# Performance work log

Hardware: AMD Instinct MI355X
Metric: run time of the kernel (lower is better)

Reference implementation:

```python
import jax, jax.numpy as jnp
import numpy as np

HDIM = 1024
N_CLASSES = 50257
CUTOFFS = [2000, 10000, N_CLASSES]  # shortlist=2000, clusters: [2000,10000), [10000,50257)
DIV = 4.0
HEAD_SIZE = CUTOFFS[0] + 2  # shortlist + 2 cluster logits


def setup_inputs() -> dict:
    key = jax.random.key(0)
    ks = jax.random.split(key, 12)
    B, S, K = 8, 512, 256
    N = B * K
    hsz0 = int(HDIM // (DIV ** 1))  # 256
    hsz1 = int(HDIM // (DIV ** 2))  # 64
    osz0 = CUTOFFS[1] - CUTOFFS[0]  # 8000
    osz1 = CUTOFFS[2] - CUTOFFS[1]  # 40257
    w = 0.02
    return {
        "targets": jax.random.randint(ks[0], (N,), 0, N_CLASSES),
        "last_hidden_states": jax.random.normal(ks[1], (B, S, HDIM), dtype=jnp.float32),
        "cls_tokens_batch": jax.random.normal(ks[2], (B, HDIM), dtype=jnp.float32),
        "idx": jax.random.randint(ks[3], (B, K), 0, S),
        "head_W": jax.random.normal(ks[4], (HEAD_SIZE, HDIM), dtype=jnp.float32) * w,
        "head_b": jnp.zeros((HEAD_SIZE,), dtype=jnp.float32),
        "proj0_W": jax.random.normal(ks[5], (hsz0, HDIM), dtype=jnp.float32) * w,
        "out0_W": jax.random.normal(ks[6], (osz0, hsz0), dtype=jnp.float32) * w,
        "proj1_W": jax.random.normal(ks[7], (hsz1, HDIM), dtype=jnp.float32) * w,
        "out1_W": jax.random.normal(ks[8], (osz1, hsz1), dtype=jnp.float32) * w,
    }


def reference(targets, last_hidden_states, cls_tokens_batch, idx,
              head_W, head_b, proj0_W, out0_W, proj1_W, out1_W):
    # Gather context token embeddings: [B, K, H] -> [N, H]
    B, S, H = last_hidden_states.shape
    x = last_hidden_states[jnp.arange(B)[:, None], idx].reshape(-1, H)
    N = x.shape[0]
    c0, c1 = CUTOFFS[0], CUTOFFS[1]

    # Head: shortlist logits + per-cluster routing logits, [N, c0+2]
    head_logprob = jax.nn.log_softmax(x @ head_W.T + head_b, axis=-1)
    # Tail clusters: low-rank projection then output GEMM + log-softmax
    lp0 = jax.nn.log_softmax((x @ proj0_W.T) @ out0_W.T, axis=-1)  # [N, 8000]
    lp1 = jax.nn.log_softmax((x @ proj1_W.T) @ out1_W.T, axis=-1)  # [N, 40257]

    n = jnp.arange(N)
    t = targets
    short = head_logprob[n, jnp.clip(t, 0, c0 - 1)]
    mid = head_logprob[:, c0] + lp0[n, jnp.clip(t - c0, 0, lp0.shape[1] - 1)]
    high = head_logprob[:, c0 + 1] + lp1[n, jnp.clip(t - c1, 0, lp1.shape[1] - 1)]
    out = jnp.where(t < c0, short, jnp.where(t < c1, mid, high))  # target log-probs [N]
    loss = -jnp.mean(out)
    return out, loss
```

## Files before the change

### kernel.cpp

```cpp
#include <hip/hip_runtime.h>
#include <hip/hip_bf16.h>

#define NROWS 2048
#define L2E 1.4426950408889634f

typedef float f32x4 __attribute__((ext_vector_type(4)));
typedef __bf16 bf16x8 __attribute__((ext_vector_type(8)));
typedef short s16x8 __attribute__((ext_vector_type(8)));

typedef const __attribute__((address_space(1))) unsigned int* gas_t;
typedef __attribute__((address_space(3))) unsigned int* las_t;

__device__ __forceinline__ unsigned short f2bf(float f) {
    unsigned int u = __float_as_uint(f);
    unsigned int r = (u + 0x7FFFu + ((u >> 16) & 1u)) >> 16;
    return (unsigned short)r;
}
__device__ __forceinline__ float bf2f(unsigned short u) {
    return __uint_as_float((unsigned int)u << 16);
}
__device__ __forceinline__ f32x4 mfma16(s16x8 a, s16x8 b, f32x4 c) {
    return __builtin_amdgcn_mfma_f32_16x16x32_bf16(
        __builtin_bit_cast(bf16x8, a), __builtin_bit_cast(bf16x8, b), c, 0, 0, 0);
}

__global__ void k_prologue(const float* __restrict__ lhs, const int* __restrict__ idx,
                           const float* __restrict__ hw, const float* __restrict__ p0w,
                           const float* __restrict__ p1w, const float* __restrict__ o0w,
                           const float* __restrict__ o1w, const float* __restrict__ hb,
                           const int* __restrict__ tgt,
                           unsigned short* __restrict__ xb, unsigned short* __restrict__ hWb,
                           unsigned short* __restrict__ pW01, unsigned short* __restrict__ o0Wb,
                           unsigned short* __restrict__ o1Wb,
                           float* __restrict__ bias_s, int* __restrict__ tc) {
    int bid = blockIdx.x;
    if (bid < 2048) {
        int tid = bid * 256 + threadIdx.x;
        int n = tid >> 8;
        int c = (tid & 255) << 2;
        int b = n >> 8, k = n & 255;
        int srow = idx[(b << 8) + k];
        const float4 v = *reinterpret_cast<const float4*>(
            lhs + (((size_t)b << 9) + srow) * 1024 + c);
        ushort4 o = make_ushort4(f2bf(v.x), f2bf(v.y), f2bf(v.z), f2bf(v.w));
        *reinterpret_cast<ushort4*>(xb + (size_t)n * 1024 + c) = o;
        return;
    }
    bid -= 2048;
    if (bid < 6968) {
        const long B0 = 2048L * 1024;
        const long B1 = B0 + 384L * 1024;
        const long B2 = B1 + 8064L * 256;
        const long B3 = B2 + 40320L * 64;
        long e = ((long)bid * 256 + threadIdx.x) * 4;
        if (e >= B3) return;
        const float* src; unsigned short* dst; long rows; int colshift; long base;
        float sc;
        if (e < B0)      { base = 0;  src = hw;  dst = hWb;  rows = 2002;  colshift = 10; sc = L2E; }
        else if (e < B1) {
            long l = e - B0;
            long row = l >> 10;
            unsigned short* d = pW01 + l;
            ushort4 o;
            if (row < 256) {
                float4 v = *reinterpret_cast<const float4*>(p0w + l);
                o = make_ushort4(f2bf(v.x), f2bf(v.y), f2bf(v.z), f2bf(v.w));
            } else if (row < 320) {
                float4 v = *reinterpret_cast<const float4*>(p1w + (l - 256L * 1024));
                o = make_ushort4(f2bf(v.x), f2bf(v.y), f2bf(v.z), f2bf(v.w));
            } else {
                o = make_ushort4(0, 0, 0, 0);
            }
            *reinterpret_cast<ushort4*>(d) = o;
            return;
        }
        else if (e < B2) { base = B1; src = o0w; dst = o0Wb; rows = 8000;  colshift = 8; sc = L2E; }
        else             { base = B2; src = o1w; dst = o1Wb; rows = 40257; colshift = 6; sc = L2E; }
        long l = e - base;
        long row = l >> colshift;
        ushort4 o;
        if (row < rows) {
            float4 v = *reinterpret_cast<const float4*>(src + l);
            o = make_ushort4(f2bf(v.x * sc), f2bf(v.y * sc), f2bf(v.z * sc), f2bf(v.w * sc));
        } else {
            o = make_ushort4(0, 0, 0, 0);
        }
        *reinterpret_cast<ushort4*>(dst + l) = o;
        return;
    }
    bid -= 6968;
    int n = bid * 256 + threadIdx.x;
    if (n >= 2048) return;
    bias_s[n] = (n < 2002) ? hb[n] * L2E : -1e30f;
    int t = tgt[n];
    tc[n] = min(t, 1999);
    tc[2048 + n] = min(max(t - 2000, 0), 7999);
    tc[4096 + n] = min(max(t - 10000, 0), 40256);
}

template <int NT>
__global__ __launch_bounds__(256)
void k_mm(const unsigned short* __restrict__ A, int lda,
          const unsigned short* __restrict__ B, int ldb,
          const float* __restrict__ bias, float* __restrict__ partial,
          unsigned short* __restrict__ hout, int hstride, int hcols, int fsplit) {
    __shared__ unsigned short As[2][128 * 64];
    __shared__ unsigned short Bs[2][128 * 64];
    const int tid = threadIdx.x;
    const int lane = tid & 63, wid = tid >> 6;
    const int wr = wid >> 1, wc = wid & 1;
    const int g = lane >> 4, cl = lane & 15;
    const int row0 = blockIdx.x * 128;
    const int col0 = blockIdx.y * 128;

    const int sr = wid * 8 + (lane >> 3);
    const int swz = ((lane & 7) ^ (lane >> 3)) * 8;
    const unsigned short* Ab = A + (size_t)(row0 + sr) * lda + swz;
    const unsigned short* Bb = B + (size_t)(col0 + sr) * ldb + swz;

    auto stage = [&](int buf, int kt) {
        const unsigned short* ga = Ab + kt;
        const unsigned short* gb = Bb + kt;
        unsigned short* la = &As[buf][wid * 8 * 64];
        unsigned short* lb = &Bs[buf][wid * 8 * 64];
#pragma unroll
        for (int i = 0; i < 4; ++i) {
            __builtin_amdgcn_global_load_lds((gas_t)(const void*)(ga + (size_t)i * 32 * lda),
                                             (las_t)(void*)(la + i * 32 * 64), 16, 0, 0);
            __builtin_amdgcn_global_load_lds((gas_t)(const void*)(gb + (size_t)i * 32 * ldb),
                                             (las_t)(void*)(lb + i * 32 * 64), 16, 0, 0);
        }
    };

    f32x4 acc[4][4] = {};
    stage(0, 0);
    asm volatile("s_waitcnt vmcnt(0)" ::: "memory");
    __builtin_amdgcn_s_barrier();
    const int sA = (cl & 7);
    for (int t = 0; t < NT; ++t) {
        if (t + 1 < NT) stage((t + 1) & 1, (t + 1) * 64);
        const unsigned short* Al = &As[t & 1][(wr * 64 + cl) * 64];
        const unsigned short* Bl = &Bs[t & 1][(wc * 64 + cl) * 64];
#pragma unroll
        for (int kk2 = 0; kk2 < 2; ++kk2) {
            const int slot = ((kk2 * 4 + g) ^ sA) * 8;
            s16x8 a[4], b[4];
#pragma unroll
            for (int mi = 0; mi < 4; ++mi)
                a[mi] = *reinterpret_cast<const s16x8*>(Al + mi * 16 * 64 + slot);
#pragma unroll
            for (int ni = 0; ni < 4; ++ni)
                b[ni] = *reinterpret_cast<const s16x8*>(Bl + ni * 16 * 64 + slot);
#pragma unroll
            for (int mi = 0; mi < 4; ++mi)
#pragma unroll
                for (int ni = 0; ni < 4; ++ni)
                    acc[mi][ni] = mfma16(a[mi], b[ni], acc[mi][ni]);
        }
        if (t + 1 < NT) {
            asm volatile("s_waitcnt vmcnt(0)" ::: "memory");
            __builtin_amdgcn_s_barrier();
        }
    }

    if ((int)blockIdx.y >= fsplit) {
        int c0 = col0 - fsplit * 128;
#pragma unroll
        for (int mi = 0; mi < 4; ++mi)
#pragma unroll
            for (int ni = 0; ni < 4; ++ni) {
                int col = c0 + wc * 64 + ni * 16 + cl;
                if (col < hcols) {
#pragma unroll
                    for (int r = 0; r < 4; ++r) {
                        int row = row0 + wr * 64 + mi * 16 + g * 4 + r;
                        hout[(size_t)row * hstride + col] = f2bf(acc[mi][ni][r]);
                    }
                }
            }
    } else {
        float bv[4];
#pragma unroll
        for (int ni = 0; ni < 4; ++ni)
            bv[ni] = bias ? bias[col0 + wc * 64 + ni * 16 + cl] : 0.f;
        int strip = blockIdx.y * 2 + wc;
#pragma unroll
        for (int mi = 0; mi < 4; ++mi)
#pragma unroll
            for (int r = 0; r < 4; ++r) {
                float s = 0.f;
#pragma unroll
                for (int ni = 0; ni < 4; ++ni)
                    s += __builtin_amdgcn_exp2f(acc[mi][ni][r] + bv[ni]);
                s += __shfl_xor(s, 1, 64);
                s += __shfl_xor(s, 2, 64);
                s += __shfl_xor(s, 4, 64);
                s += __shfl_xor(s, 8, 64);
                if (cl == 0)
                    partial[(size_t)strip * NROWS + row0 + wr * 64 + mi * 16 + g * 4 + r] = s;
            }
    }
}

#define OUT1_IT 5
__global__ __launch_bounds__(256, 4)
void k_out1(const unsigned short* __restrict__ h01, const unsigned short* __restrict__ B,
            float* __restrict__ p1) {
    __shared__ unsigned short Bs[2][128 * 64];
    const int tid = threadIdx.x;
    const int lane = tid & 63, wid = tid >> 6;
    const int wr = wid >> 1, wc = wid & 1;
    const int g = lane >> 4, cl = lane & 15;
    const int row0 = blockIdx.x * 128 + wr * 64;
    const int t0 = blockIdx.y * OUT1_IT;

    s16x8 a[4][2];
#pragma unroll
    for (int mi = 0; mi < 4; ++mi)
#pragma unroll
        for (int kk = 0; kk < 2; ++kk)
            a[mi][kk] = *reinterpret_cast<const s16x8*>(
                h01 + (size_t)(row0 + mi * 16 + cl) * 320 + 256 + kk * 32 + g * 8);

    const int sr = wid * 8 + (lane >> 3);
    const int swz = ((lane & 7) ^ (lane >> 3)) * 8;
    auto stage = [&](int buf, int tile) {
        const unsigned short* gb = B + ((size_t)tile * 128 + sr) * 64 + swz;
        unsigned short* lb = &Bs[buf][wid * 8 * 64];
#pragma unroll
        for (int i = 0; i < 4; ++i)
            __builtin_amdgcn_global_load_lds((gas_t)(const void*)(gb + (size_t)i * 32 * 64),
                                             (las_t)(void*)(lb + i * 32 * 64), 16, 0, 0);
    };

    float sexp[4][4] = {};
    const f32x4 z4 = {0.f, 0.f, 0.f, 0.f};
    stage(0, t0);
    asm volatile("s_waitcnt vmcnt(0)" ::: "memory");
    __builtin_amdgcn_s_barrier();
    int buf = 0;
    const int sA = (cl & 7);
#pragma unroll 1
    for (int it = 0; it < OUT1_IT; ++it) {
        if (it + 1 < OUT1_IT) stage(buf ^ 1, t0 + it + 1);
        const unsigned short* Bl = Bs[buf];
#pragma unroll
        for (int ni = 0; ni < 4; ++ni) {
            const unsigned short* br = Bl + (wc * 64 + ni * 16 + cl) * 64;
            s16x8 b0 = *reinterpret_cast<const s16x8*>(br + (g ^ sA) * 8);
            s16x8 b1 = *reinterpret_cast<const s16x8*>(br + ((4 + g) ^ sA) * 8);
            f32x4 acc[4];
#pragma unroll
            for (int mi = 0; mi < 4; ++mi)
                acc[mi] = mfma16(a[mi][0], b0, z4);
#pragma unroll
            for (int mi = 0; mi < 4; ++mi)
                acc[mi] = mfma16(a[mi][1], b1, acc[mi]);
#pragma unroll
            for (int mi = 0; mi < 4; ++mi)
#pragma unroll
                for (int r = 0; r < 4; ++r)
                    sexp[mi][r] += __builtin_amdgcn_exp2f(acc[mi][r]);
        }
        if (it + 1 < OUT1_IT) {
            asm volatile("s_waitcnt vmcnt(0)" ::: "memory");
            __builtin_amdgcn_s_barrier();
            buf ^= 1;
        }
    }

#pragma unroll
    for (int mi = 0; mi < 4; ++mi)
#pragma unroll
        for (int r = 0; r < 4; ++r) {
            float s = sexp[mi][r];
            s += __shfl_xor(s, 1, 64);
            s += __shfl_xor(s, 2, 64);
            s += __shfl_xor(s, 4, 64);
            s += __shfl_xor(s, 8, 64);
            if (cl == 0)
                p1[(size_t)(blockIdx.y * 2 + wc) * NROWS + row0 + mi * 16 + g * 4 + r] = s;
        }
}

__global__ __launch_bounds__(256)
void k_dots(const unsigned short* __restrict__ xb, const unsigned short* __restrict__ h01,
            const float* __restrict__ headW, const float* __restrict__ hb,
            const float* __restrict__ o0w, const float* __restrict__ o1w,
            const int* __restrict__ tc,
            float* __restrict__ tgh, float* __restrict__ r0, float* __restrict__ r1,
            float* __restrict__ tg0, float* __restrict__ tg1) {
    int lane = threadIdx.x & 63;
    int n = (blockIdx.x * 256 + threadIdx.x) >> 6;
    int tch = tc[n], tc0 = tc[2048 + n], tc1 = tc[4096 + n];
    const unsigned short* xr = xb + (size_t)n * 1024 + lane * 16;
    s16x8 x0 = *reinterpret_cast<const s16x8*>(xr);
    s16x8 x1 = *reinterpret_cast<const s16x8*>(xr + 8);
    const float* wh = headW + (size_t)tch * 1024 + lane * 16;
    const float* wa = headW + (size_t)2000 * 1024 + lane * 16;
    const float* wb = headW + (size_t)2001 * 1024 + lane * 16;
    float dh = 0.f, da = 0.f, db = 0.f;
#pragma unroll
    for (int i = 0; i < 8; ++i) {
        float xv = bf2f((unsigned short)x0[i]);
        dh += xv * wh[i]; da += xv * wa[i]; db += xv * wb[i];
    }
#pragma unroll
    for (int i = 0; i < 8; ++i) {
        float xv = bf2f((unsigned short)x1[i]);
        dh += xv * wh[8 + i]; da += xv * wa[8 + i]; db += xv * wb[8 + i];
    }
    ushort4 h0v = *reinterpret_cast<const ushort4*>(h01 + (size_t)n * 320 + lane * 4);
    float4 w0v = *reinterpret_cast<const float4*>(o0w + (size_t)tc0 * 256 + lane * 4);
    float d2 = bf2f(h0v.x) * w0v.x + bf2f(h0v.y) * w0v.y +
               bf2f(h0v.z) * w0v.z + bf2f(h0v.w) * w0v.w;
    float d3 = bf2f(h01[(size_t)n * 320 + 256 + lane]) * o1w[(size_t)tc1 * 64 + lane];
#pragma unroll
    for (int m = 1; m < 64; m <<= 1) {
        dh += __shfl_xor(dh, m, 64);
        da += __shfl_xor(da, m, 64);
        db += __shfl_xor(db, m, 64);
        d2 += __shfl_xor(d2, m, 64);
        d3 += __shfl_xor(d3, m, 64);
    }
    if (lane == 0) {
        tgh[n] = dh + hb[tch];
        r0[n] = da + hb[2000];
        r1[n] = db + hb[2001];
        tg0[n] = d2;
        tg1[n] = d3;
    }
}

__global__ void k_finalize(const float* __restrict__ ph, const float* __restrict__ p0,
                           const float* __restrict__ p1, const float* __restrict__ tgh,
                           const float* __restrict__ r0, const float* __restrict__ r1,
                           const float* __restrict__ tg0, const float* __restrict__ tg1,
                           const int* __restrict__ tgt, float* __restrict__ outv,
                           float* __restrict__ bsum) {
    int n = blockIdx.x * 128 + threadIdx.x;
    float sh = 0.f, s0 = 0.f, s1 = 0.f;
    for (int s = 0; s < 32; ++s) sh += ph[(size_t)s * NROWS + n];
    for (int s = 0; s < 126; ++s) s0 += p0[(size_t)s * NROWS + n];
    for (int s = 0; s < 126; ++s) s1 += p1[(size_t)s * NROWS + n];
    s0 -= 64.f;
    s1 -= 63.f;
    float lh = __logf(sh), l0 = __logf(s0), l1 = __logf(s1);
    int t = tgt[n];
    float o;
    if (t < 2000) o = tgh[n] - lh;
    else if (t < 10000) o = (r0[n] - lh) + (tg0[n] - l0);
    else o = (r1[n] - lh) + (tg1[n] - l1);
    outv[n] = o;
    __shared__ float red[128];
    red[threadIdx.x] = o;
    __syncthreads();
    for (int s = 64; s > 0; s >>= 1) {
        if (threadIdx.x < s) red[threadIdx.x] += red[threadIdx.x + s];
        __syncthreads();
    }
    if (threadIdx.x == 0) bsum[blockIdx.x] = red[0];
}

__global__ void k_loss(const float* __restrict__ bsum, float* __restrict__ loss) {
    float s = 0.f;
    for (int i = 0; i < 16; ++i) s += bsum[i];
    *loss = -s / (float)NROWS;
}

extern "C" void kernel_launch(void* const* d_in, const int* in_sizes, int n_in,
                              void* d_out, int out_size, void* d_ws, size_t ws_size,
                              hipStream_t stream) {
    const int* targets   = (const int*)d_in[0];
    const float* lhs     = (const float*)d_in[1];
    const int* idx       = (const int*)d_in[3];
    const float* head_W  = (const float*)d_in[4];
    const float* head_b  = (const float*)d_in[5];
    const float* proj0_W = (const float*)d_in[6];
    const float* out0_W  = (const float*)d_in[7];
    const float* proj1_W = (const float*)d_in[8];
    const float* out1_W  = (const float*)d_in[9];

    char* ws = (char*)d_ws;
    size_t off = 0;
    auto alloc = [&](size_t bytes) -> void* {
        void* p = ws + off;
        off += (bytes + 255) & ~(size_t)255;
        return p;
    };

    unsigned short* xb   = (unsigned short*)alloc((size_t)2048 * 1024 * 2);
    unsigned short* wB   = (unsigned short*)alloc((size_t)2432 * 1024 * 2);
    unsigned short* hWb  = wB;
    unsigned short* pW01 = wB + (size_t)2048 * 1024;
    unsigned short* o0Wb = (unsigned short*)alloc((size_t)8064 * 256 * 2);
    unsigned short* o1Wb = (unsigned short*)alloc((size_t)40320 * 64 * 2);
    unsigned short* h01  = (unsigned short*)alloc((size_t)2048 * 320 * 2);
    float* ph  = (float*)alloc((size_t)32 * 2048 * 4);
    float* p0  = (float*)alloc((size_t)126 * 2048 * 4);
    float* p1  = (float*)alloc((size_t)126 * 2048 * 4);
    float* tgh = (float*)alloc(2048 * 4);
    float* r0  = (float*)alloc(2048 * 4);
    float* r1  = (float*)alloc(2048 * 4);
    float* tg0 = (float*)alloc(2048 * 4);
    float* tg1 = (float*)alloc(2048 * 4);
    int*   tc  = (int*)alloc(3 * 2048 * 4);
    float* bias_s = (float*)alloc(2048 * 4);
    float* bsum = (float*)alloc(16 * 4);

    k_prologue<<<9024, 256, 0, stream>>>(lhs, idx, head_W, proj0_W, proj1_W, out0_W, out1_W,
                                         head_b, targets,
                                         xb, hWb, pW01, o0Wb, o1Wb, bias_s, tc);

    k_mm<16><<<dim3(16, 19), 256, 0, stream>>>(
        xb, 1024, wB, 1024, bias_s, ph, h01, 320, 320, 16);
    k_mm<4><<<dim3(16, 63), 256, 0, stream>>>(
        h01, 320, o0Wb, 256, nullptr, p0, nullptr, 0, 0, 63);
    k_out1<<<dim3(16, 63), 256, 0, stream>>>(h01, o1Wb, p1);

    k_dots<<<512, 256, 0, stream>>>(xb, h01, head_W, head_b, out0_W, out1_W, tc,
                                    tgh, r0, r1, tg0, tg1);

    float* outv = (float*)d_out;
    float* loss = (float*)d_out + NROWS;
    k_finalize<<<16, 128, 0, stream>>>(ph, p0, p1, tgh, r0, r1, tg0, tg1, targets, outv, bsum);
    k_loss<<<1, 1, 0, stream>>>(bsum, loss);
}
```

Measured before the change: 92.39 us.

## Merge out0 GEMM, out1 GEMM and target-dot kernels into one launch

Three independent kernels (the cluster-0 GEMM with exp-sum, the cluster-1 GEMM with exp-sum, and the per-row target dot products) become a single kernel that dispatches on block index into three roles. This removes two launch gaps and lets the three workloads' blocks run concurrently, filling the GPU better than three serial launches with tails. In exchange the merged kernel uses 32 KB of shared memory and the register budget of the heaviest branch, and the launch-bounds occupancy hint of 4 blocks per SM is dropped, which may lower occupancy for the out1 path.

```diff
diff --git a/kernel.cpp b/kernel.cpp
--- a/kernel.cpp
+++ b/kernel.cpp
@@ -203,95 +203,163 @@
 }
 
 #define OUT1_IT 5
-__global__ __launch_bounds__(256, 4)
-void k_out1(const unsigned short* __restrict__ h01, const unsigned short* __restrict__ B,
-            float* __restrict__ p1) {
-    __shared__ unsigned short Bs[2][128 * 64];
+__global__ __launch_bounds__(256)
+void k_tail(const unsigned short* __restrict__ h01, const unsigned short* __restrict__ o0Wb,
+            const unsigned short* __restrict__ o1Wb, const unsigned short* __restrict__ xb,
+            const float* __restrict__ headW, const float* __restrict__ hb,
+            const float* __restrict__ o0w, const float* __restrict__ o1w,
+            const int* __restrict__ tc,
+            float* __restrict__ p0, float* __restrict__ p1,
+            float* __restrict__ tgh, float* __restrict__ r0, float* __restrict__ r1,
+            float* __restrict__ tg0, float* __restrict__ tg1) {
+    __shared__ unsigned short smem[4][128 * 64];
     const int tid = threadIdx.x;
     const int lane = tid & 63, wid = tid >> 6;
     const int wr = wid >> 1, wc = wid & 1;
     const int g = lane >> 4, cl = lane & 15;
-    const int row0 = blockIdx.x * 128 + wr * 64;
-    const int t0 = blockIdx.y * OUT1_IT;
-
-    s16x8 a[4][2];
-#pragma unroll
-    for (int mi = 0; mi < 4; ++mi)
-#pragma unroll
-        for (int kk = 0; kk < 2; ++kk)
-            a[mi][kk] = *reinterpret_cast<const s16x8*>(
-                h01 + (size_t)(row0 + mi * 16 + cl) * 320 + 256 + kk * 32 + g * 8);
-
-    const int sr = wid * 8 + (lane >> 3);
-    const int swz = ((lane & 7) ^ (lane >> 3)) * 8;
-    auto stage = [&](int buf, int tile) {
-        const unsigned short* gb = B + ((size_t)tile * 128 + sr) * 64 + swz;
-        unsigned short* lb = &Bs[buf][wid * 8 * 64];
-#pragma unroll
-        for (int i = 0; i < 4; ++i)
-            __builtin_amdgcn_global_load_lds((gas_t)(const void*)(gb + (size_t)i * 32 * 64),
-                                             (las_t)(void*)(lb + i * 32 * 64), 16, 0, 0);
-    };
-
-    float sexp[4][4] = {};
-    const f32x4 z4 = {0.f, 0.f, 0.f, 0.f};
-    stage(0, t0);
-    asm volatile("s_waitcnt vmcnt(0)" ::: "memory");
-    __builtin_amdgcn_s_barrier();
-    int buf = 0;
-    const int sA = (cl & 7);
+    int bid = blockIdx.x;
+
+    if (bid < 1008) {
+        const int row0 = (bid & 15) * 128;
+        const int col0 = (bid >> 4) * 128;
+        const int sr = wid * 8 + (lane >> 3);
+        const int swz = ((lane & 7) ^ (lane >> 3)) * 8;
+        const unsigned short* Ab = h01 + (size_t)(row0 + sr) * 320 + swz;
+        const unsigned short* Bb = o0Wb + (size_t)(col0 + sr) * 256 + swz;
+        auto stage = [&](int buf, int kt) {
+            const unsigned short* ga = Ab + kt;
+            const unsigned short* gb = Bb + kt;
+            unsigned short* la = &smem[buf][wid * 8 * 64];
+            unsigned short* lb = &smem[2 + buf][wid * 8 * 64];
+#pragma unroll
+            for (int i = 0; i < 4; ++i) {
+                __builtin_amdgcn_global_load_lds((gas_t)(const void*)(ga + (size_t)i * 32 * 320),
+                                                 (las_t)(void*)(la + i * 32 * 64), 16, 0, 0);
+                __builtin_amdgcn_global_load_lds((gas_t)(const void*)(gb + (size_t)i * 32 * 256),
+                                                 (las_t)(void*)(lb + i * 32 * 64), 16, 0, 0);
+            }
+        };
+        f32x4 acc[4][4] = {};
+        stage(0, 0);
+        asm volatile("s_waitcnt vmcnt(0)" ::: "memory");
+        __builtin_amdgcn_s_barrier();
+        const int sA = (cl & 7);
+        for (int t = 0; t < 4; ++t) {
+            if (t < 3) stage((t + 1) & 1, (t + 1) * 64);
+            const unsigned short* Al = &smem[t & 1][(wr * 64 + cl) * 64];
+            const unsigned short* Bl = &smem[2 + (t & 1)][(wc * 64 + cl) * 64];
+#pragma unroll
+            for (int kk2 = 0; kk2 < 2; ++kk2) {
+                const int slot = ((kk2 * 4 + g) ^ sA) * 8;
+                s16x8 a[4], b[4];
+#pragma unroll
+                for (int mi = 0; mi < 4; ++mi)
+                    a[mi] = *reinterpret_cast<const s16x8*>(Al + mi * 16 * 64 + slot);
+#pragma unroll
+                for (int ni = 0; ni < 4; ++ni)
+                    b[ni] = *reinterpret_cast<const s16x8*>(Bl + ni * 16 * 64 + slot);
+#pragma unroll
+                for (int mi = 0; mi < 4; ++mi)
+#pragma unroll
+                    for (int ni = 0; ni < 4; ++ni)
+                        acc[mi][ni] = mfma16(a[mi], b[ni], acc[mi][ni]);
+            }
+            if (t < 3) {
+                asm volatile("s_waitcnt vmcnt(0)" ::: "memory");
+                __builtin_amdgcn_s_barrier();
+            }
+        }
+        int strip = (bid >> 4) * 2 + wc;
+#pragma unroll
+        for (int mi = 0; mi < 4; ++mi)
+#pragma unroll
+            for (int r = 0; r < 4; ++r) {
+                float s = 0.f;
+#pragma unroll
+                for (int ni = 0; ni < 4; ++ni)
+                    s += __builtin_amdgcn_exp2f(acc[mi][ni][r]);
+                s += __shfl_xor(s, 1, 64);
+                s += __shfl_xor(s, 2, 64);
+                s += __shfl_xor(s, 4, 64);
+                s += __shfl_xor(s, 8, 64);
+                if (cl == 0)
+                    p0[(size_t)strip * NROWS + row0 + wr * 64 + mi * 16 + g * 4 + r] = s;
+            }
+        return;
+    }
+    if (bid < 2016) {
+        bid -= 1008;
+        const int row0 = (bid & 15) * 128 + wr * 64;
+        const int yb = bid >> 4;
+        const int t0 = yb * OUT1_IT;
+        s16x8 a[4][2];
+#pragma unroll
+        for (int mi = 0; mi < 4; ++mi)
+#pragma unroll
+            for (int kk = 0; kk < 2; ++kk)
+                a[mi][kk] = *reinterpret_cast<const s16x8*>(
+                    h01 + (size_t)(row0 + mi * 16 + cl) * 320 + 256 + kk * 32 + g * 8);
+        const int sr = wid * 8 + (lane >> 3);
+        const int swz = ((lane & 7) ^ (lane >> 3)) * 8;
+        auto stage = [&](int buf, int tile) {
+            const unsigned short* gb = o1Wb + ((size_t)tile * 128 + sr) * 64 + swz;
+            unsigned short* lb = &smem[buf][wid * 8 * 64];
+#pragma unroll
+            for (int i = 0; i < 4; ++i)
+                __builtin_amdgcn_global_load_lds((gas_t)(const void*)(gb + (size_t)i * 32 * 64),
+                                                 (las_t)(void*)(lb + i * 32 * 64), 16, 0, 0);
+        };
+        float sexp[4][4] = {};
+        const f32x4 z4 = {0.f, 0.f, 0.f, 0.f};
+        stage(0, t0);
+        asm volatile("s_waitcnt vmcnt(0)" ::: "memory");
+        __builtin_amdgcn_s_barrier();
+        int buf = 0;
+        const int sA = (cl & 7);
 #pragma unroll 1
-    for (int it = 0; it < OUT1_IT; ++it) {
-        if (it + 1 < OUT1_IT) stage(buf ^ 1, t0 + it + 1);
-        const unsigned short* Bl = Bs[buf];
-#pragma unroll
-        for (int ni = 0; ni < 4; ++ni) {
-            const unsigned short* br = Bl + (wc * 64 + ni * 16 + cl) * 64;
-            s16x8 b0 = *reinterpret_cast<const s16x8*>(br + (g ^ sA) * 8);
-            s16x8 b1 = *reinterpret_cast<const s16x8*>(br + ((4 + g) ^ sA) * 8);
-            f32x4 acc[4];
-#pragma unroll
-            for (int mi = 0; mi < 4; ++mi)
-                acc[mi] = mfma16(a[mi][0], b0, z4);
-#pragma unroll
-            for (int mi = 0; mi < 4; ++mi)
-                acc[mi] = mfma16(a[mi][1], b1, acc[mi]);
-#pragma unroll
-            for (int mi = 0; mi < 4; ++mi)
-#pragma unroll
-                for (int r = 0; r < 4; ++r)
-                    sexp[mi][r] += __builtin_amdgcn_exp2f(acc[mi][r]);
-        }
-        if (it + 1 < OUT1_IT) {
-            asm volatile("s_waitcnt vmcnt(0)" ::: "memory");
-            __builtin_amdgcn_s_barrier();
-            buf ^= 1;
-        }
-    }
-
-#pragma unroll
-    for (int mi = 0; mi < 4; ++mi)
-#pragma unroll
-        for (int r = 0; r < 4; ++r) {
-            float s = sexp[mi][r];
-            s += __shfl_xor(s, 1, 64);
-            s += __shfl_xor(s, 2, 64);
-            s += __shfl_xor(s, 4, 64);
-            s += __shfl_xor(s, 8, 64);
-            if (cl == 0)
-                p1[(size_t)(blockIdx.y * 2 + wc) * NROWS + row0 + mi * 16 + g * 4 + r] = s;
-        }
-}
-
-__global__ __launch_bounds__(256)
-void k_dots(const unsigned short* __restrict__ xb, const unsigned short* __restrict__ h01,
-            const float* __restrict__ headW, const float* __restrict__ hb,
-            const float* __restrict__ o0w, const float* __restrict__ o1w,
-            const int* __restrict__ tc,
-            float* __restrict__ tgh, float* __restrict__ r0, float* __restrict__ r1,
-            float* __restrict__ tg0, float* __restrict__ tg1) {
-    int lane = threadIdx.x & 63;
-    int n = (blockIdx.x * 256 + threadIdx.x) >> 6;
+        for (int it = 0; it < OUT1_IT; ++it) {
+            if (it + 1 < OUT1_IT) stage(buf ^ 1, t0 + it + 1);
+            const unsigned short* Bl = smem[buf];
+#pragma unroll
+            for (int ni = 0; ni < 4; ++ni) {
+                const unsigned short* br = Bl + (wc * 64 + ni * 16 + cl) * 64;
+                s16x8 b0 = *reinterpret_cast<const s16x8*>(br + (g ^ sA) * 8);
+                s16x8 b1 = *reinterpret_cast<const s16x8*>(br + ((4 + g) ^ sA) * 8);
+                f32x4 acc[4];
+#pragma unroll
+                for (int mi = 0; mi < 4; ++mi)
+                    acc[mi] = mfma16(a[mi][0], b0, z4);
+#pragma unroll
+                for (int mi = 0; mi < 4; ++mi)
+                    acc[mi] = mfma16(a[mi][1], b1, acc[mi]);
+#pragma unroll
+                for (int mi = 0; mi < 4; ++mi)
+#pragma unroll
+                    for (int r = 0; r < 4; ++r)
+                        sexp[mi][r] += __builtin_amdgcn_exp2f(acc[mi][r]);
+            }
+            if (it + 1 < OUT1_IT) {
+                asm volatile("s_waitcnt vmcnt(0)" ::: "memory");
+                __builtin_amdgcn_s_barrier();
+                buf ^= 1;
+            }
+        }
+#pragma unroll
+        for (int mi = 0; mi < 4; ++mi)
+#pragma unroll
+            for (int r = 0; r < 4; ++r) {
+                float s = sexp[mi][r];
+                s += __shfl_xor(s, 1, 64);
+                s += __shfl_xor(s, 2, 64);
+                s += __shfl_xor(s, 4, 64);
+                s += __shfl_xor(s, 8, 64);
+                if (cl == 0)
+                    p1[(size_t)(yb * 2 + wc) * NROWS + row0 + mi * 16 + g * 4 + r] = s;
+            }
+        return;
+    }
+    bid -= 2016;
+    int n = (bid * 256 + tid) >> 6;
     int tch = tc[n], tc0 = tc[2048 + n], tc1 = tc[4096 + n];
     const unsigned short* xr = xb + (size_t)n * 1024 + lane * 16;
     s16x8 x0 = *reinterpret_cast<const s16x8*>(xr);
@@ -414,12 +482,9 @@
 
     k_mm<16><<<dim3(16, 19), 256, 0, stream>>>(
         xb, 1024, wB, 1024, bias_s, ph, h01, 320, 320, 16);
-    k_mm<4><<<dim3(16, 63), 256, 0, stream>>>(
-        h01, 320, o0Wb, 256, nullptr, p0, nullptr, 0, 0, 63);
-    k_out1<<<dim3(16, 63), 256, 0, stream>>>(h01, o1Wb, p1);
-
-    k_dots<<<512, 256, 0, stream>>>(xb, h01, head_W, head_b, out0_W, out1_W, tc,
-                                    tgh, r0, r1, tg0, tg1);
+
+    k_tail<<<2528, 256, 0, stream>>>(h01, o0Wb, o1Wb, xb, head_W, head_b, out0_W, out1_W,
+                                     tc, p0, p1, tgh, r0, r1, tg0, tg1);
 
     float* outv = (float*)d_out;
     float* loss = (float*)d_out + NROWS;
```

After: 87.53 us. 1.06x faster.
